# Kernel tuning notes

Measured on AMD Instinct MI355X. Metric: run time of the kernel, lower is better.

Reference implementation:

```python
import jax, jax.numpy as jnp
import numpy as np

B, K, M, MN = 256, 32, 64, 256
E, H, Q = 128, 128, 128
NE, NR, NNODES = 100000, 500, 256  # entities, relations, max_nodes


def setup_inputs() -> dict:
    key = jax.random.key(0)
    ks = jax.random.split(key, 24)
    f = lambda k, s: jax.random.normal(k, s, jnp.float32) * 0.05
    inp = {}
    inp['start_entities'] = jax.random.randint(ks[0], (B,), 0, NE)
    inp['aims'] = jax.random.randint(ks[1], (B, K), 0, NE)
    inp['node_pos'] = jnp.broadcast_to(jnp.arange(1, K + 1, dtype=jnp.int32), (B, K))
    inp['neighbor_nodes'] = jax.random.randint(ks[2], (B, K, M), 0, NNODES)
    inp['neighbor_relations'] = jax.random.randint(ks[3], (B, K, M), 0, NR)
    inp['neighbors_num'] = jax.random.randint(ks[4], (B, K), 0, M + 1)
    inp['currents'] = jax.random.randint(ks[5], (B,), 0, NNODES)
    inp['candidate_nodes'] = jax.random.randint(ks[6], (B, MN), 0, NNODES)
    inp['candidate_entities'] = jax.random.randint(ks[7], (B, MN), 0, NE)
    inp['candidate_relations'] = jax.random.randint(ks[8], (B, MN), 0, NR)
    inp['candidate_masks'] = jax.random.randint(ks[9], (B, MN), 0, 2).astype(bool)
    inp['entity_emb'] = f(ks[10], (NE, E))
    inp['relation_emb'] = f(ks[11], (NR, E))
    inp['hidden_W'] = f(ks[12], (H, E)); inp['hidden_b'] = f(ks[13], (H,))
    inp['pass_W'] = f(ks[14], (H, H + E)); inp['pass_b'] = f(ks[15], (H,))
    inp['nexthop_W'] = f(ks[16], (H, H + Q)); inp['nexthop_b'] = f(ks[17], (H,))
    inp['candidate_W'] = f(ks[18], (H, H + 2 * E)); inp['candidate_b'] = f(ks[19], (H,))
    inp['gate_W'] = f(ks[20], (1, H + Q)); inp['gate_b'] = f(ks[21], (1,))
    inp['query'] = f(ks[22], (B, Q))
    return inp


def _linear(x, W, b):
    return x @ W.T + b


def _lrelu(x):
    return jax.nn.leaky_relu(x, 0.01)  # torch LeakyReLU default


def _gather_nodes(node_emb, idx):
    # node_emb: (B, N+2, H), idx: (B, ...) -> (B, ..., H)
    b = node_emb.shape[0]
    g = jnp.take_along_axis(node_emb, idx.reshape(b, -1)[:, :, None], axis=1)
    return g.reshape(*idx.shape, node_emb.shape[-1])


def reference(start_entities, aims, node_pos, neighbor_nodes, neighbor_relations,
              neighbors_num, currents, candidate_nodes, candidate_entities,
              candidate_relations, candidate_masks, entity_emb, relation_emb,
              hidden_W, hidden_b, pass_W, pass_b, nexthop_W, nexthop_b,
              candidate_W, candidate_b, gate_W, gate_b, query):
    # ---- Agent.init ----
    node_emb = jnp.zeros((B, NNODES + 2, H), jnp.float32)
    init = _lrelu(_linear(entity_emb[start_entities], hidden_W, hidden_b))
    node_emb = node_emb.at[:, 0].set(init)
    # ---- Agent.aggregate: gather -> Linear -> masked mean -> scatter ----
    aim_e = entity_emb[aims]                                   # (B,K,E)
    nb_node = _gather_nodes(node_emb, neighbor_nodes)          # (B,K,M,H)
    nb_rel = relation_emb[neighbor_relations]                  # (B,K,M,E)
    nb = _linear(jnp.concatenate([nb_node, nb_rel], -1), pass_W, pass_b)  # pass_activation = identity
    keep = jnp.arange(M) < neighbors_num[:, :, None]           # (B,K,M)
    nb = jnp.where(keep[..., None], nb, 0.0)
    denom = (neighbors_num + (neighbors_num == 0)).astype(jnp.float32)
    agg = nb.sum(axis=2) / denom[..., None]                    # (B,K,H)
    upd = _lrelu(_linear(aim_e, hidden_W, hidden_b) + agg)
    node_emb = node_emb.at[jnp.arange(B)[:, None], node_pos].set(upd)
    # ---- Agent.next_hop ----
    cur = _gather_nodes(node_emb, currents)                    # (B,H)
    cur_cat = jnp.concatenate([cur, query], axis=1)            # (B,H+Q)
    state = _lrelu(_linear(cur_cat, nexthop_W, nexthop_b))     # (B,H)
    cnode = _gather_nodes(node_emb, candidate_nodes)           # (B,MN,H)
    cand = _lrelu(_linear(jnp.concatenate(
        [cnode, entity_emb[candidate_entities], relation_emb[candidate_relations]], -1),
        candidate_W, candidate_b))                             # (B,MN,H)
    thresh = _linear(cur_cat, gate_W, gate_b)                  # (B,1)
    scores = jnp.einsum('bh,bmh->bm', state, cand) / jnp.sqrt(jnp.float32(E))
    scores = jnp.where(candidate_masks, scores, jnp.float32(-100000.0))
    final_scores = jnp.concatenate([scores, thresh], axis=1)   # (B,MN+1)
    return final_scores
```

## Files before the change

### kernel.cpp

```cpp
#include <hip/hip_runtime.h>

#define B 256
#define K 32
#define M 64
#define MN 256
#define E 128
#define H 128
#define Q 128
#define NSLOT 258
#define CTILE 32
#define XPAD 392

typedef __attribute__((ext_vector_type(8))) short short8;
typedef __attribute__((ext_vector_type(4))) short short4b;
typedef __attribute__((ext_vector_type(4))) float f32x4;

__device__ __forceinline__ float lrelu(float x){ return x >= 0.f ? x : 0.01f*x; }

__device__ __forceinline__ unsigned short f2bf(float f){
    unsigned int u = __float_as_uint(f);
    unsigned int r = u + 0x7FFFu + ((u >> 16) & 1u);
    return (unsigned short)(r >> 16);
}

__device__ __forceinline__ short4b pack4(float4 v){
    short4b r;
    r.x = (short)f2bf(v.x); r.y = (short)f2bf(v.y);
    r.z = (short)f2bf(v.z); r.w = (short)f2bf(v.w);
    return r;
}

__global__ void k_front(const int* __restrict__ aims, const int* __restrict__ nbr_nodes,
                        const int* __restrict__ nbr_rels, const int* __restrict__ nbr_num,
                        const int* __restrict__ start_ent, const int* __restrict__ node_pos,
                        const float* __restrict__ ent_emb, const float* __restrict__ rel_emb,
                        const float* __restrict__ hW, const float* __restrict__ hb,
                        const float* __restrict__ passW, const float* __restrict__ candW,
                        unsigned short* __restrict__ Xg, float* __restrict__ ab,
                        int* __restrict__ map,
                        float* __restrict__ init_out, float* __restrict__ wninit_out,
                        unsigned short* __restrict__ Wf, unsigned short* __restrict__ Wcatf){
    int blk = blockIdx.x, t = threadIdx.x;
    __shared__ float e[128];
    __shared__ float si[128];

    if (blk < (B*K)/4) {
        int w = t >> 6, lane = t & 63;
        int bk = blk*4 + w;
        int num = nbr_num[bk];
        int sidx = nbr_rels[(long)bk*M + lane];
        int nn   = nbr_nodes[(long)bk*M + lane];
        unsigned long long mask = __ballot((lane < num) && (nn == 0));
        int c0 = (int)__popcll(mask);
        float denom = (float)(num > 0 ? num : 1);
        float ax = 0.f, ay = 0.f;
        int m = 0;
        for (; m + 4 <= num; m += 4) {
            int r0 = __shfl(sidx, m+0), r1 = __shfl(sidx, m+1);
            int r2 = __shfl(sidx, m+2), r3 = __shfl(sidx, m+3);
            float2 v0 = *(const float2*)&rel_emb[(long)r0*E + lane*2];
            float2 v1 = *(const float2*)&rel_emb[(long)r1*E + lane*2];
            float2 v2 = *(const float2*)&rel_emb[(long)r2*E + lane*2];
            float2 v3 = *(const float2*)&rel_emb[(long)r3*E + lane*2];
            ax += v0.x + v1.x + v2.x + v3.x;
            ay += v0.y + v1.y + v2.y + v3.y;
        }
        for (; m < num; ++m) {
            int r = __shfl(sidx, m);
            float2 v = *(const float2*)&rel_emb[(long)r*E + lane*2];
            ax += v.x; ay += v.y;
        }
        ushort2 rp; rp.x = f2bf(ax/denom); rp.y = f2bf(ay/denom);
        *(ushort2*)&Xg[(long)bk*256 + lane*2] = rp;
        float2 av = *(const float2*)&ent_emb[(long)aims[bk]*E + lane*2];
        ushort2 apk; apk.x = f2bf(av.x); apk.y = f2bf(av.y);
        *(ushort2*)&Xg[(long)bk*256 + 128 + lane*2] = apk;
        if (lane == 0) {
            ab[bk*2+0] = (float)c0 / denom;
            ab[bk*2+1] = (float)num / denom;
        }
        return;
    }

    int pb = blk - (B*K)/4;
    if (pb < 256) {
        int b = pb;
        if (t < 128) e[t] = ent_emb[(long)start_ent[b]*E + t];
        __syncthreads();
        if (t < 128) {
            float acc = hb[t];
            #pragma unroll 8
            for (int j=0;j<E;j++) acc += hW[t*E+j]*e[j];
            float v = lrelu(acc);
            si[t] = v;
            init_out[b*H+t] = v;
        }
        __syncthreads();
        if (t < 128) {
            float acc2 = 0.f;
            #pragma unroll 8
            for (int j=0;j<H;j++) acc2 += passW[t*(H+E)+j]*si[j];
            wninit_out[b*H+t] = acc2;
        }
    } else if (pb < 512) {
        int b = pb - 256;
        for (int i=t;i<NSLOT;i+=256) map[b*NSLOT+i] = -2;
        __syncthreads();
        if (t==0) map[b*NSLOT+0] = -1;
        __syncthreads();
        if (t<K) map[b*NSLOT + node_pos[b*K+t]] = t;
    } else if (pb < 704) {
        int i = (pb-512)*256 + t;
        int j = i & 7;
        int l = (i >> 3) & 63;
        int ct = (i >> 9) & 1;
        int r = i >> 10;
        int ks = r % 12, w = r / 12;
        int row = w*32 + ct*16 + (l & 15);
        int col = ks*32 + (l >> 4)*8 + j;
        Wf[i] = f2bf(candW[row*384 + col]);
    } else {
        int i = (pb-704)*256 + t;
        int j = i & 7;
        int l = (i >> 3) & 63;
        int ct = (i >> 9) & 1;
        int r = i >> 10;
        int ks = r & 7, w = r >> 3;
        int row = w*32 + ct*16 + (l & 15);
        int col = ks*32 + (l >> 4)*8 + j;
        float v = (col < 128) ? passW[row*256 + 128 + col] : hW[row*128 + (col-128)];
        Wcatf[i] = f2bf(v);
    }
}

__global__ void k_updg(const unsigned short* __restrict__ Xg, const float* __restrict__ ab,
                       const unsigned short* __restrict__ Wcatf,
                       const float* __restrict__ hb_, const float* __restrict__ passb,
                       const float* __restrict__ wninit,
                       float* __restrict__ upd){
    int b = blockIdx.x;
    int t = threadIdx.x;
    __shared__ __align__(16) unsigned short Xs[32][264];
    __shared__ float wni[128];
    __shared__ float sab[64];
    #pragma unroll
    for (int it = 0; it < 4; it++) {
        int idx = it*256 + t;
        int r = idx >> 5;
        int cc = (idx & 31) * 8;
        *(short8*)&Xs[r][cc] = *(const short8*)&Xg[((long)b*32 + r)*256 + cc];
    }
    if (t < 128) wni[t] = wninit[b*128 + t];
    else if (t < 192) sab[t-128] = ab[b*64 + (t-128)];

    int w    = t >> 6;
    int lane = t & 63;
    int l16  = lane & 15;
    int lhi  = lane >> 4;
    int hbase = w*32;

    short8 bw[8][2];
    #pragma unroll
    for (int ks = 0; ks < 8; ks++) {
        #pragma unroll
        for (int ct = 0; ct < 2; ct++)
            bw[ks][ct] = *(const short8*)&Wcatf[((((w*8+ks)*2+ct)*64) + lane)*8];
    }
    __syncthreads();

    f32x4 acc[2][2];
    #pragma unroll
    for (int rt=0;rt<2;rt++)
        #pragma unroll
        for (int ct=0;ct<2;ct++)
            acc[rt][ct] = (f32x4){0.f,0.f,0.f,0.f};

    #pragma unroll
    for (int ks = 0; ks < 8; ks++) {
        int kof = ks*32 + lhi*8;
        short8 a0 = *(const short8*)&Xs[l16][kof];
        short8 a1 = *(const short8*)&Xs[16 + l16][kof];
        acc[0][0] = __builtin_amdgcn_mfma_f32_16x16x32_bf16(a0, bw[ks][0], acc[0][0], 0, 0, 0);
        acc[0][1] = __builtin_amdgcn_mfma_f32_16x16x32_bf16(a0, bw[ks][1], acc[0][1], 0, 0, 0);
        acc[1][0] = __builtin_amdgcn_mfma_f32_16x16x32_bf16(a1, bw[ks][0], acc[1][0], 0, 0, 0);
        acc[1][1] = __builtin_amdgcn_mfma_f32_16x16x32_bf16(a1, bw[ks][1], acc[1][1], 0, 0, 0);
    }

    int h0 = hbase + l16, h1 = hbase + 16 + l16;
    float hb0 = hb_[h0], hb1 = hb_[h1];
    float pb0 = passb[h0], pb1 = passb[h1];
    float w0 = wni[h0],  w1 = wni[h1];
    #pragma unroll
    for (int rt=0; rt<2; rt++) {
        #pragma unroll
        for (int i=0;i<4;i++) {
            int r = rt*16 + 4*lhi + i;
            float al = sab[r*2], be = sab[r*2+1];
            upd[((long)b*32 + r)*128 + h0] = lrelu(hb0 + al*w0 + be*pb0 + acc[rt][0][i]);
            upd[((long)b*32 + r)*128 + h1] = lrelu(hb1 + al*w1 + be*pb1 + acc[rt][1][i]);
        }
    }
}

__global__ void k_state(const int* __restrict__ currents, const int* __restrict__ map,
                        const float* __restrict__ init, const float* __restrict__ upd,
                        const float* __restrict__ query,
                        const float* __restrict__ nW, const float* __restrict__ nb,
                        const float* __restrict__ gW, const float* __restrict__ gb,
                        float* __restrict__ state, float* __restrict__ out){
    int b = blockIdx.x, t = threadIdx.x;
    __shared__ float cc[H+Q];
    __shared__ float wsum[2];
    int mv = map[b*NSLOT + currents[b]];
    float cv = 0.f;
    if (mv == -1) cv = init[b*H+t];
    else if (mv >= 0) cv = upd[((long)b*K+mv)*H + t];
    cc[t] = cv;
    cc[H+t] = query[b*Q+t];
    __syncthreads();
    float acc = nb[t];
    #pragma unroll 8
    for (int j=0;j<H+Q;j++) acc += nW[t*(H+Q)+j]*cc[j];
    state[b*H+t] = lrelu(acc);
    float tv = gW[t]*cc[t] + gW[H+t]*cc[H+t];
    for (int off=32; off>0; off>>=1) tv += __shfl_down(tv, off);
    if ((t&63)==0) wsum[t>>6] = tv;
    __syncthreads();
    if (t==0) out[b*(MN+1) + MN] = wsum[0] + wsum[1] + gb[0];
}

__global__ void k_cand(const int* __restrict__ cnodes, const int* __restrict__ cents,
                       const int* __restrict__ crels, const int* __restrict__ cmask,
                       const int* __restrict__ map,
                       const float* __restrict__ init, const float* __restrict__ upd,
                       const float* __restrict__ ent_emb, const float* __restrict__ rel_emb,
                       const unsigned short* __restrict__ Wf, const float* __restrict__ cb,
                       const float* __restrict__ state,
                       float* __restrict__ out){
    int blk = blockIdx.x;
    int b  = blk >> 3;
    int c0 = (blk & 7) * CTILE;
    int t  = threadIdx.x;

    __shared__ __align__(16) unsigned short Xb[CTILE][XPAD];
    __shared__ float sscore[4][CTILE];
    __shared__ int sce[CTILE], scr[CTILE], smv[CTILE];

    if (t < CTILE) {
        int row = b*MN + c0 + t;
        int cn = cnodes[row];
        sce[t] = cents[row];
        scr[t] = crels[row];
        smv[t] = map[b*NSLOT + cn];
    }
    __syncthreads();

    {
        int c8 = t >> 5;
        int q  = t & 31;
        #pragma unroll
        for (int i = 0; i < 4; i++) {
            int c = i*8 + c8;
            int mv = smv[c];
            float4 nv = {0.f,0.f,0.f,0.f};
            if (mv == -1)      nv = *(const float4*)&init[b*H + q*4];
            else if (mv >= 0)  nv = *(const float4*)&upd[((long)b*K+mv)*H + q*4];
            float4 ev = *(const float4*)&ent_emb[(long)sce[c]*E + q*4];
            float4 rv = *(const float4*)&rel_emb[(long)scr[c]*E + q*4];
            *(short4b*)&Xb[c][q*4]        = pack4(nv);
            *(short4b*)&Xb[c][128 + q*4]  = pack4(ev);
            *(short4b*)&Xb[c][256 + q*4]  = pack4(rv);
        }
    }

    int w    = t >> 6;
    int lane = t & 63;
    int l16  = lane & 15;
    int lhi  = lane >> 4;

    short8 bw[12][2];
    #pragma unroll
    for (int ks = 0; ks < 12; ks++) {
        #pragma unroll
        for (int ct = 0; ct < 2; ct++)
            bw[ks][ct] = *(const short8*)&Wf[((((w*12+ks)*2+ct)*64) + lane)*8];
    }
    float s0 = state[b*H + w*32 + l16];
    float s1 = state[b*H + w*32 + 16 + l16];
    float cb0 = cb[w*32 + l16];
    float cb1 = cb[w*32 + 16 + l16];
    __syncthreads();

    f32x4 acc[2][2];
    #pragma unroll
    for (int rt=0;rt<2;rt++)
        #pragma unroll
        for (int ct=0;ct<2;ct++)
            acc[rt][ct] = (f32x4){0.f,0.f,0.f,0.f};

    #pragma unroll
    for (int ks = 0; ks < 12; ks++) {
        int kof = ks*32 + lhi*8;
        short8 a0 = *(const short8*)&Xb[l16][kof];
        short8 a1 = *(const short8*)&Xb[16 + l16][kof];
        acc[0][0] = __builtin_amdgcn_mfma_f32_16x16x32_bf16(a0, bw[ks][0], acc[0][0], 0, 0, 0);
        acc[0][1] = __builtin_amdgcn_mfma_f32_16x16x32_bf16(a0, bw[ks][1], acc[0][1], 0, 0, 0);
        acc[1][0] = __builtin_amdgcn_mfma_f32_16x16x32_bf16(a1, bw[ks][0], acc[1][0], 0, 0, 0);
        acc[1][1] = __builtin_amdgcn_mfma_f32_16x16x32_bf16(a1, bw[ks][1], acc[1][1], 0, 0, 0);
    }

    #pragma unroll
    for (int rt=0; rt<2; rt++) {
        float ps[4];
        #pragma unroll
        for (int i=0;i<4;i++)
            ps[i] = lrelu(acc[rt][0][i] + cb0)*s0 + lrelu(acc[rt][1][i] + cb1)*s1;
        #pragma unroll
        for (int msk=1; msk<16; msk<<=1) {
            #pragma unroll
            for (int i=0;i<4;i++) ps[i] += __shfl_xor(ps[i], msk);
        }
        if (l16 == 0) {
            #pragma unroll
            for (int i=0;i<4;i++)
                sscore[w][rt*16 + 4*lhi + i] = ps[i];
        }
    }
    __syncthreads();

    if (t < CTILE) {
        int row = b*MN + c0 + t;
        float s = (sscore[0][t] + sscore[1][t] + sscore[2][t] + sscore[3][t])
                  * 0.08838834764831845f;
        out[b*(MN+1) + c0 + t] = cmask[row] ? s : -100000.0f;
    }
}

extern "C" void kernel_launch(void* const* d_in, const int* in_sizes, int n_in,
                              void* d_out, int out_size, void* d_ws, size_t ws_size,
                              hipStream_t stream){
    (void)in_sizes; (void)n_in; (void)out_size; (void)ws_size;
    const int* start_entities      = (const int*)d_in[0];
    const int* aims                = (const int*)d_in[1];
    const int* node_pos            = (const int*)d_in[2];
    const int* neighbor_nodes      = (const int*)d_in[3];
    const int* neighbor_relations  = (const int*)d_in[4];
    const int* neighbors_num       = (const int*)d_in[5];
    const int* currents            = (const int*)d_in[6];
    const int* candidate_nodes     = (const int*)d_in[7];
    const int* candidate_entities  = (const int*)d_in[8];
    const int* candidate_relations = (const int*)d_in[9];
    const int* candidate_masks     = (const int*)d_in[10];
    const float* entity_emb   = (const float*)d_in[11];
    const float* relation_emb = (const float*)d_in[12];
    const float* hidden_W     = (const float*)d_in[13];
    const float* hidden_b     = (const float*)d_in[14];
    const float* pass_W       = (const float*)d_in[15];
    const float* pass_b       = (const float*)d_in[16];
    const float* nexthop_W    = (const float*)d_in[17];
    const float* nexthop_b    = (const float*)d_in[18];
    const float* candidate_W  = (const float*)d_in[19];
    const float* candidate_b  = (const float*)d_in[20];
    const float* gate_W       = (const float*)d_in[21];
    const float* gate_b       = (const float*)d_in[22];
    const float* query        = (const float*)d_in[23];
    float* out = (float*)d_out;

    float* ws     = (float*)d_ws;
    float* init   = ws;
    float* wninit = init + B*H;
    float* upd    = wninit + B*H;
    float* state  = upd + (long)B*K*H;
    float* ab     = state + B*H;
    int*   map    = (int*)(ab + B*K*2);
    unsigned short* Wf    = (unsigned short*)(map + B*NSLOT);
    unsigned short* Wcatf = Wf + 49152;
    unsigned short* Xg    = Wcatf + 32768;

    k_front<<<(B*K)/4 + 832, 256, 0, stream>>>(aims, neighbor_nodes, neighbor_relations,
                                               neighbors_num, start_entities, node_pos,
                                               entity_emb, relation_emb,
                                               hidden_W, hidden_b, pass_W, candidate_W,
                                               Xg, ab, map, init, wninit, Wf, Wcatf);
    k_updg<<<B, 256, 0, stream>>>(Xg, ab, Wcatf, hidden_b, pass_b, wninit, upd);
    k_state<<<B, 128, 0, stream>>>(currents, map, init, upd, query,
                                   nexthop_W, nexthop_b, gate_W, gate_b, state, out);
    k_cand<<<B*(MN/CTILE), 256, 0, stream>>>(candidate_nodes, candidate_entities,
                                             candidate_relations, candidate_masks,
                                             map, init, upd, entity_emb, relation_emb,
                                             Wf, candidate_b, state, out);
}
```

Baseline: 56.92 us.

## Loop k_cand over four candidate tiles per block to reuse register weights

k_cand now runs 2 blocks per batch row, each looping over four 32-candidate tiles, so the 24 short8 weight fragments loaded into registers are reused four times instead of being reloaded by eight separate blocks. It adds launch_bounds(256,2). k_front reorders its block ranges so the 832 weight/init blocks come first, and the relation-gather loop is unrolled to 8. The tile loop serialises gather and MFMA work inside each block and cuts the grid from 2048 to 512 blocks, which may reduce latency hiding.

After: 56.53 us. No clear change (-0.7%).

```diff
diff --git a/kernel.cpp b/kernel.cpp
--- a/kernel.cpp
+++ b/kernel.cpp
@@ -44,9 +44,9 @@
     __shared__ float e[128];
     __shared__ float si[128];
 
-    if (blk < (B*K)/4) {
+    if (blk >= 832) {
         int w = t >> 6, lane = t & 63;
-        int bk = blk*4 + w;
+        int bk = (blk - 832)*4 + w;
         int num = nbr_num[bk];
         int sidx = nbr_rels[(long)bk*M + lane];
         int nn   = nbr_nodes[(long)bk*M + lane];
@@ -55,15 +55,21 @@
         float denom = (float)(num > 0 ? num : 1);
         float ax = 0.f, ay = 0.f;
         int m = 0;
-        for (; m + 4 <= num; m += 4) {
+        for (; m + 8 <= num; m += 8) {
             int r0 = __shfl(sidx, m+0), r1 = __shfl(sidx, m+1);
             int r2 = __shfl(sidx, m+2), r3 = __shfl(sidx, m+3);
+            int r4 = __shfl(sidx, m+4), r5 = __shfl(sidx, m+5);
+            int r6 = __shfl(sidx, m+6), r7 = __shfl(sidx, m+7);
             float2 v0 = *(const float2*)&rel_emb[(long)r0*E + lane*2];
             float2 v1 = *(const float2*)&rel_emb[(long)r1*E + lane*2];
             float2 v2 = *(const float2*)&rel_emb[(long)r2*E + lane*2];
             float2 v3 = *(const float2*)&rel_emb[(long)r3*E + lane*2];
-            ax += v0.x + v1.x + v2.x + v3.x;
-            ay += v0.y + v1.y + v2.y + v3.y;
+            float2 v4 = *(const float2*)&rel_emb[(long)r4*E + lane*2];
+            float2 v5 = *(const float2*)&rel_emb[(long)r5*E + lane*2];
+            float2 v6 = *(const float2*)&rel_emb[(long)r6*E + lane*2];
+            float2 v7 = *(const float2*)&rel_emb[(long)r7*E + lane*2];
+            ax += (v0.x + v1.x) + (v2.x + v3.x) + (v4.x + v5.x) + (v6.x + v7.x);
+            ay += (v0.y + v1.y) + (v2.y + v3.y) + (v4.y + v5.y) + (v6.y + v7.y);
         }
         for (; m < num; ++m) {
             int r = __shfl(sidx, m);
@@ -82,7 +88,7 @@
         return;
     }
 
-    int pb = blk - (B*K)/4;
+    int pb = blk;
     if (pb < 256) {
         int b = pb;
         if (t < 128) e[t] = ent_emb[(long)start_ent[b]*E + t];
@@ -229,54 +235,37 @@
     if (t==0) out[b*(MN+1) + MN] = wsum[0] + wsum[1] + gb[0];
 }
 
-__global__ void k_cand(const int* __restrict__ cnodes, const int* __restrict__ cents,
-                       const int* __restrict__ crels, const int* __restrict__ cmask,
-                       const int* __restrict__ map,
-                       const float* __restrict__ init, const float* __restrict__ upd,
-                       const float* __restrict__ ent_emb, const float* __restrict__ rel_emb,
-                       const unsigned short* __restrict__ Wf, const float* __restrict__ cb,
-                       const float* __restrict__ state,
-                       float* __restrict__ out){
+__global__ __launch_bounds__(256, 2)
+void k_cand(const int* __restrict__ cnodes, const int* __restrict__ cents,
+            const int* __restrict__ crels, const int* __restrict__ cmask,
+            const int* __restrict__ map,
+            const float* __restrict__ init, const float* __restrict__ upd,
+            const float* __restrict__ ent_emb, const float* __restrict__ rel_emb,
+            const unsigned short* __restrict__ Wf, const float* __restrict__ cb,
+            const float* __restrict__ state,
+            float* __restrict__ out){
     int blk = blockIdx.x;
-    int b  = blk >> 3;
-    int c0 = (blk & 7) * CTILE;
+    int b  = blk >> 1;
+    int cbase = (blk & 1) * 128;
     int t  = threadIdx.x;
 
     __shared__ __align__(16) unsigned short Xb[CTILE][XPAD];
     __shared__ float sscore[4][CTILE];
-    __shared__ int sce[CTILE], scr[CTILE], smv[CTILE];
-
-    if (t < CTILE) {
-        int row = b*MN + c0 + t;
-        int cn = cnodes[row];
+    __shared__ int sce[128], scr[128], smv[128];
+
+    if (t < 128) {
+        int row = b*MN + cbase + t;
         sce[t] = cents[row];
         scr[t] = crels[row];
-        smv[t] = map[b*NSLOT + cn];
-    }
-    __syncthreads();
-
-    {
-        int c8 = t >> 5;
-        int q  = t & 31;
-        #pragma unroll
-        for (int i = 0; i < 4; i++) {
-            int c = i*8 + c8;
-            int mv = smv[c];
-            float4 nv = {0.f,0.f,0.f,0.f};
-            if (mv == -1)      nv = *(const float4*)&init[b*H + q*4];
-            else if (mv >= 0)  nv = *(const float4*)&upd[((long)b*K+mv)*H + q*4];
-            float4 ev = *(const float4*)&ent_emb[(long)sce[c]*E + q*4];
-            float4 rv = *(const float4*)&rel_emb[(long)scr[c]*E + q*4];
-            *(short4b*)&Xb[c][q*4]        = pack4(nv);
-            *(short4b*)&Xb[c][128 + q*4]  = pack4(ev);
-            *(short4b*)&Xb[c][256 + q*4]  = pack4(rv);
-        }
+        smv[t] = map[b*NSLOT + cnodes[row]];
     }
 
     int w    = t >> 6;
     int lane = t & 63;
     int l16  = lane & 15;
     int lhi  = lane >> 4;
+    int c8   = t >> 5;
+    int q    = t & 31;
 
     short8 bw[12][2];
     #pragma unroll
@@ -285,54 +274,73 @@
         for (int ct = 0; ct < 2; ct++)
             bw[ks][ct] = *(const short8*)&Wf[((((w*12+ks)*2+ct)*64) + lane)*8];
     }
-    float s0 = state[b*H + w*32 + l16];
-    float s1 = state[b*H + w*32 + 16 + l16];
+    float s0  = state[b*H + w*32 + l16];
+    float s1  = state[b*H + w*32 + 16 + l16];
     float cb0 = cb[w*32 + l16];
     float cb1 = cb[w*32 + 16 + l16];
     __syncthreads();
 
-    f32x4 acc[2][2];
-    #pragma unroll
-    for (int rt=0;rt<2;rt++)
-        #pragma unroll
-        for (int ct=0;ct<2;ct++)
-            acc[rt][ct] = (f32x4){0.f,0.f,0.f,0.f};
-
-    #pragma unroll
-    for (int ks = 0; ks < 12; ks++) {
-        int kof = ks*32 + lhi*8;
-        short8 a0 = *(const short8*)&Xb[l16][kof];
-        short8 a1 = *(const short8*)&Xb[16 + l16][kof];
-        acc[0][0] = __builtin_amdgcn_mfma_f32_16x16x32_bf16(a0, bw[ks][0], acc[0][0], 0, 0, 0);
-        acc[0][1] = __builtin_amdgcn_mfma_f32_16x16x32_bf16(a0, bw[ks][1], acc[0][1], 0, 0, 0);
-        acc[1][0] = __builtin_amdgcn_mfma_f32_16x16x32_bf16(a1, bw[ks][0], acc[1][0], 0, 0, 0);
-        acc[1][1] = __builtin_amdgcn_mfma_f32_16x16x32_bf16(a1, bw[ks][1], acc[1][1], 0, 0, 0);
-    }
-
-    #pragma unroll
-    for (int rt=0; rt<2; rt++) {
-        float ps[4];
-        #pragma unroll
-        for (int i=0;i<4;i++)
-            ps[i] = lrelu(acc[rt][0][i] + cb0)*s0 + lrelu(acc[rt][1][i] + cb1)*s1;
-        #pragma unroll
-        for (int msk=1; msk<16; msk<<=1) {
+    #pragma unroll
+    for (int tile = 0; tile < 4; ++tile) {
+        #pragma unroll
+        for (int i = 0; i < 4; i++) {
+            int ci = tile*32 + i*8 + c8;
+            int cl = i*8 + c8;
+            int mv = smv[ci];
+            float4 nv = {0.f,0.f,0.f,0.f};
+            if (mv == -1)      nv = *(const float4*)&init[b*H + q*4];
+            else if (mv >= 0)  nv = *(const float4*)&upd[((long)b*K+mv)*H + q*4];
+            float4 ev = *(const float4*)&ent_emb[(long)sce[ci]*E + q*4];
+            float4 rv = *(const float4*)&rel_emb[(long)scr[ci]*E + q*4];
+            *(short4b*)&Xb[cl][q*4]       = pack4(nv);
+            *(short4b*)&Xb[cl][128 + q*4] = pack4(ev);
+            *(short4b*)&Xb[cl][256 + q*4] = pack4(rv);
+        }
+        __syncthreads();
+
+        f32x4 acc[2][2];
+        #pragma unroll
+        for (int rt=0;rt<2;rt++)
             #pragma unroll
-            for (int i=0;i<4;i++) ps[i] += __shfl_xor(ps[i], msk);
-        }
-        if (l16 == 0) {
+            for (int ct=0;ct<2;ct++)
+                acc[rt][ct] = (f32x4){0.f,0.f,0.f,0.f};
+
+        #pragma unroll
+        for (int ks = 0; ks < 12; ks++) {
+            int kof = ks*32 + lhi*8;
+            short8 a0 = *(const short8*)&Xb[l16][kof];
+            short8 a1 = *(const short8*)&Xb[16 + l16][kof];
+            acc[0][0] = __builtin_amdgcn_mfma_f32_16x16x32_bf16(a0, bw[ks][0], acc[0][0], 0, 0, 0);
+            acc[0][1] = __builtin_amdgcn_mfma_f32_16x16x32_bf16(a0, bw[ks][1], acc[0][1], 0, 0, 0);
+            acc[1][0] = __builtin_amdgcn_mfma_f32_16x16x32_bf16(a1, bw[ks][0], acc[1][0], 0, 0, 0);
+            acc[1][1] = __builtin_amdgcn_mfma_f32_16x16x32_bf16(a1, bw[ks][1], acc[1][1], 0, 0, 0);
+        }
+
+        #pragma unroll
+        for (int rt=0; rt<2; rt++) {
+            float ps[4];
             #pragma unroll
             for (int i=0;i<4;i++)
-                sscore[w][rt*16 + 4*lhi + i] = ps[i];
-        }
-    }
-    __syncthreads();
-
-    if (t < CTILE) {
-        int row = b*MN + c0 + t;
-        float s = (sscore[0][t] + sscore[1][t] + sscore[2][t] + sscore[3][t])
-                  * 0.08838834764831845f;
-        out[b*(MN+1) + c0 + t] = cmask[row] ? s : -100000.0f;
+                ps[i] = lrelu(acc[rt][0][i] + cb0)*s0 + lrelu(acc[rt][1][i] + cb1)*s1;
+            #pragma unroll
+            for (int msk=1; msk<16; msk<<=1) {
+                #pragma unroll
+                for (int i=0;i<4;i++) ps[i] += __shfl_xor(ps[i], msk);
+            }
+            if (l16 == 0) {
+                #pragma unroll
+                for (int i=0;i<4;i++)
+                    sscore[w][rt*16 + 4*lhi + i] = ps[i];
+            }
+        }
+        __syncthreads();
+
+        if (t < CTILE) {
+            int row = b*MN + cbase + tile*32 + t;
+            float s = (sscore[0][t] + sscore[1][t] + sscore[2][t] + sscore[3][t])
+                      * 0.08838834764831845f;
+            out[b*(MN+1) + cbase + tile*32 + t] = cmask[row] ? s : -100000.0f;
+        }
     }
 }
 
@@ -377,7 +385,7 @@
     unsigned short* Wcatf = Wf + 49152;
     unsigned short* Xg    = Wcatf + 32768;
 
-    k_front<<<(B*K)/4 + 832, 256, 0, stream>>>(aims, neighbor_nodes, neighbor_relations,
+    k_front<<<832 + (B*K)/4, 256, 0, stream>>>(aims, neighbor_nodes, neighbor_relations,
                                                neighbors_num, start_entities, node_pos,
                                                entity_emb, relation_emb,
                                                hidden_W, hidden_b, pass_W, candidate_W,
@@ -385,8 +393,8 @@
     k_updg<<<B, 256, 0, stream>>>(Xg, ab, Wcatf, hidden_b, pass_b, wninit, upd);
     k_state<<<B, 128, 0, stream>>>(currents, map, init, upd, query,
                                    nexthop_W, nexthop_b, gate_W, gate_b, state, out);
-    k_cand<<<B*(MN/CTILE), 256, 0, stream>>>(candidate_nodes, candidate_entities,
-                                             candidate_relations, candidate_masks,
-                                             map, init, upd, entity_emb, relation_emb,
-                                             Wf, candidate_b, state, out);
-}
+    k_cand<<<2*B, 256, 0, stream>>>(candidate_nodes, candidate_entities,
+                                    candidate_relations, candidate_masks,
+                                    map, init, upd, entity_emb, relation_emb,
+                                    Wf, candidate_b, state, out);
+}
```
